# Performance work log

Hardware: AMD Instinct MI355X
Metric: run time of the kernel (lower is better)

Reference implementation:

```python
import jax, jax.numpy as jnp
import numpy as np

N = 50000      # nodes
E = 1600000    # edges (avg degree 32)
F = 11         # atom_features
ED = 4         # edge_dim
L = 4          # num_layers
G = 500        # graphs in batch


def _lin(k, fi, fo, layers=True):
    s = 1.0 / np.sqrt(fi)
    kw, kb = jax.random.split(k)
    sw = (L, fi, fo) if layers else (fi, fo)
    sb = (L, fo) if layers else (fo,)
    return (jax.random.uniform(kw, sw, jnp.float32, -s, s),
            jax.random.uniform(kb, sb, jnp.float32, -s, s))


def setup_inputs() -> dict:
    key = jax.random.key(0)
    ks = jax.random.split(key, 16)
    inp = {}
    inp["h"] = jax.random.normal(ks[0], (N, F), jnp.float32)
    inp["pos"] = jax.random.normal(ks[1], (N, 3), jnp.float32)
    inp["edge_index"] = jax.random.randint(ks[2], (2, E), 0, N)
    inp["edge_attr"] = jax.random.normal(ks[3], (E, ED), jnp.float32)
    inp["batch"] = jnp.sort(jax.random.randint(ks[4], (N,), 0, G))
    # stacked per-layer linear params
    specs = [("W_msg1", "b_msg1", 2 * F + 1 + ED, F),
             ("W_msg2", "b_msg2", F, F),
             ("W_attn", "b_attn", F, 1),
             ("W_upd1", "b_upd1", 2 * F, F),
             ("W_upd2", "b_upd2", F, F),
             ("W_x1", "b_x1", 2 * F + 1 + ED, F),
             ("W_x2", "b_x2", F, F),
             ("W_x3", "b_x3", F, 1)]
    for i, (wn, bn, fi, fo) in enumerate(specs):
        w, b = _lin(ks[5 + i], fi, fo)
        inp[wn] = w
        inp[bn] = b
    w, b = _lin(ks[14], F, 1, layers=False)
    inp["W_pred"] = w
    inp["b_pred"] = b
    return inp


def reference(h, pos, edge_index, edge_attr, batch,
              W_msg1, b_msg1, W_msg2, b_msg2, W_attn, b_attn,
              W_upd1, b_upd1, W_upd2, b_upd2,
              W_x1, b_x1, W_x2, b_x2, W_x3, b_x3,
              W_pred, b_pred):
    src, dst = edge_index[0], edge_index[1]  # j (source), i (target)
    x = pos
    for l in range(L):
        h_i, h_j = h[dst], h[src]
        x_i, x_j = x[dst], x[src]
        d = jnp.linalg.norm(x_j - x_i, axis=-1, keepdims=True)  # [E,1]
        feat = jnp.concatenate([h_i, h_j, d * d, edge_attr], axis=-1)  # [E,27]
        m = jax.nn.silu(feat @ W_msg1[l] + b_msg1[l])
        m = jax.nn.silu(m @ W_msg2[l] + b_msg2[l])
        attn = jax.nn.sigmoid(m @ W_attn[l] + b_attn[l])
        msg_h = attn * m                                          # [E,F]
        phi = jax.nn.silu(feat @ W_x1[l] + b_x1[l])
        phi = jax.nn.silu(phi @ W_x2[l] + b_x2[l])
        phi = phi @ W_x3[l] + b_x3[l]                             # [E,1]
        msg_x = (x_i - x_j) / (d + 1.0) * phi                     # [E,3]
        agg_h = jax.ops.segment_sum(msg_h, dst, num_segments=N)
        agg_x = jax.ops.segment_sum(msg_x, dst, num_segments=N)
        upd = jax.nn.silu(jnp.concatenate([h, agg_h], axis=-1) @ W_upd1[l] + b_upd1[l])
        upd = upd @ W_upd2[l] + b_upd2[l]
        h = h + upd          # residual (h = h + h_upd in outer loop)
        x = x + agg_x        # out_x = x + agg_x
    # global mean pool over graphs, then linear head
    counts = jax.ops.segment_sum(jnp.ones((N, 1), h.dtype), batch, num_segments=G)
    h_graph = jax.ops.segment_sum(h, batch, num_segments=G) / jnp.maximum(counts, 1.0)
    return (h_graph @ W_pred + b_pred).reshape(-1)
```

## Files before the change

kernel.cpp:

```cpp
#include <hip/hip_runtime.h>

#define N_NODES 50000
#define N_EDGES 1600000
#define F 11
#define FEAT 27
#define NLAYERS 4
#define NGRAPH 500
#define NVALS 14
#define PRESTRIDE 24
#define NBLK 196

__device__ __forceinline__ float siluf(float v) { return v * (1.0f / (1.0f + __expf(-v))); }
__device__ __forceinline__ float sigmf(float v) { return 1.0f / (1.0f + __expf(-v)); }

__device__ __forceinline__ float2 pkfma(float2 a, float2 b, float2 c) {
    float2 d;
    asm("v_pk_fma_f32 %0, %1, %2, %3" : "=v"(d) : "v"(a), "v"(b), "v"(c));
    return d;
}
__device__ __forceinline__ void rank1_pk(float v, const float4 w, float2& a0, float2& a1) {
    float2 vv = make_float2(v, v);
    a0 = pkfma(vv, make_float2(w.x, w.y), a0);
    a1 = pkfma(vv, make_float2(w.z, w.w), a1);
}

__global__ __launch_bounds__(256) void hist_kernel(const int* __restrict__ dst,
                                                   int* __restrict__ deg) {
    int e = blockIdx.x * 256 + threadIdx.x;
    if (e < N_EDGES) atomicAdd(&deg[dst[e]], 1);
}

__global__ __launch_bounds__(256) void scan1_kernel(const int* __restrict__ deg,
                                                    int* __restrict__ part,
                                                    int* __restrict__ bsum) {
    int t = threadIdx.x;
    int i = blockIdx.x * 256 + t;
    int v = (i < N_NODES) ? deg[i] : 0;
    int lane = t & 63, wid = t >> 6;
    int s = v;
    #pragma unroll
    for (int off = 1; off < 64; off <<= 1) {
        int u = __shfl_up(s, off);
        if (lane >= off) s += u;
    }
    __shared__ int wsum[4];
    if (lane == 63) wsum[wid] = s;
    __syncthreads();
    int wpre = 0;
    #pragma unroll
    for (int w = 0; w < 4; ++w) if (w < wid) wpre += wsum[w];
    if (i < N_NODES) part[i] = s + wpre - v;
    if (t == 255) bsum[blockIdx.x] = s + wpre;
}

__global__ __launch_bounds__(256) void scan2_kernel(int* __restrict__ bsum) {
    int t = threadIdx.x;
    int v = (t < NBLK) ? bsum[t] : 0;
    int lane = t & 63, wid = t >> 6;
    int s = v;
    #pragma unroll
    for (int off = 1; off < 64; off <<= 1) {
        int u = __shfl_up(s, off);
        if (lane >= off) s += u;
    }
    __shared__ int wsum[4];
    if (lane == 63) wsum[wid] = s;
    __syncthreads();
    int wpre = 0;
    #pragma unroll
    for (int w = 0; w < 4; ++w) if (w < wid) wpre += wsum[w];
    if (t < NBLK) bsum[t] = s + wpre - v;
}

__global__ __launch_bounds__(256) void scan3_kernel(const int* __restrict__ part,
                                                    const int* __restrict__ bsum,
                                                    int* __restrict__ cursor) {
    int i = blockIdx.x * 256 + threadIdx.x;
    if (i < N_NODES) cursor[i] = part[i] + bsum[blockIdx.x];
}

__global__ __launch_bounds__(256) void scatter_perm(const int* __restrict__ dst,
                                                    int* __restrict__ cursor,
                                                    int* __restrict__ perm) {
    int e = blockIdx.x * 256 + threadIdx.x;
    if (e >= N_EDGES) return;
    int d = dst[e];
    int pos = atomicAdd(&cursor[d], 1);
    perm[pos] = e;
}

__global__ __launch_bounds__(256) void mat_kernel(
    const int* __restrict__ perm, const int* __restrict__ src,
    const int* __restrict__ dst, const float4* __restrict__ eattr4,
    int* __restrict__ ssrc, int* __restrict__ sdst, float4* __restrict__ sea) {
    int i = blockIdx.x * 256 + threadIdx.x;
    if (i >= N_EDGES) return;
    int e = perm[i];
    ssrc[i] = src[e];
    sdst[i] = dst[e];
    sea[i] = eattr4[e];
}

__global__ __launch_bounds__(256) void init_kernel(
    const float* __restrict__ h0, const float* __restrict__ pos,
    float* __restrict__ h, float* __restrict__ x,
    const float* __restrict__ Wm1, const float* __restrict__ bm1,
    const float* __restrict__ Wx1, const float* __restrict__ bx1,
    float* __restrict__ preA, float* __restrict__ preB)
{
    __shared__ float sM[2 * F * F], sX[2 * F * F], sbm[F], sbx[F];
    int t = threadIdx.x;
    for (int i2 = t; i2 < 2 * F * F; i2 += 256) { sM[i2] = Wm1[i2]; sX[i2] = Wx1[i2]; }
    if (t < F) { sbm[t] = bm1[t]; sbx[t] = bx1[t]; }
    __syncthreads();

    int n = blockIdx.x * 256 + t;
    if (n >= N_NODES) return;

    float hv[F];
    #pragma unroll
    for (int f2 = 0; f2 < F; ++f2) { hv[f2] = h0[n * F + f2]; h[n * F + f2] = hv[f2]; }
    #pragma unroll
    for (int k = 0; k < 3; ++k) x[n * 3 + k] = pos[n * 3 + k];

    float am[F], bm_[F], ax[F], bx_[F];
    #pragma unroll
    for (int o = 0; o < F; ++o) { am[o] = sbm[o]; ax[o] = sbx[o]; bm_[o] = 0.f; bx_[o] = 0.f; }
    #pragma unroll
    for (int fi = 0; fi < F; ++fi) {
        float v = hv[fi];
        #pragma unroll
        for (int o = 0; o < F; ++o) {
            am[o]  = fmaf(v, sM[fi * F + o], am[o]);
            bm_[o] = fmaf(v, sM[(F + fi) * F + o], bm_[o]);
            ax[o]  = fmaf(v, sX[fi * F + o], ax[o]);
            bx_[o] = fmaf(v, sX[(F + fi) * F + o], bx_[o]);
        }
    }
    #pragma unroll
    for (int o = 0; o < F; ++o) {
        preA[n * PRESTRIDE + o]      = am[o];
        preA[n * PRESTRIDE + 12 + o] = ax[o];
        preB[n * PRESTRIDE + o]      = bm_[o];
        preB[n * PRESTRIDE + 12 + o] = bx_[o];
    }
    preA[n * PRESTRIDE + 11] = 0.f; preA[n * PRESTRIDE + 23] = 0.f;
    preB[n * PRESTRIDE + 11] = 0.f; preB[n * PRESTRIDE + 23] = 0.f;
}

__global__ __launch_bounds__(256) void edge_kernel(
    const float* __restrict__ preA, const float* __restrict__ preB,
    const float* __restrict__ x,
    const int* __restrict__ ssrc, const int* __restrict__ sdst,
    const float4* __restrict__ sea,
    const float* __restrict__ Wm1,
    const float* __restrict__ Wm2, const float* __restrict__ bm2,
    const float* __restrict__ Wa,  const float* __restrict__ ba,
    const float* __restrict__ Wx1,
    const float* __restrict__ Wx2, const float* __restrict__ bx2,
    const float* __restrict__ Wx3, const float* __restrict__ bx3,
    float* __restrict__ agg_h, float* __restrict__ agg_x)
{
    __shared__ float4 sW2m[F * 3], sW2x[F * 3];
    __shared__ float4 sD2m[3], sD2x[3], sEAm[4 * 3], sEAx[4 * 3];
    __shared__ float4 sB2m[3], sB2x[3], sWav[3], sWx3v[3];
    __shared__ float sba, sbx3;
    int t = threadIdx.x;
    {
        float* w2m = (float*)sW2m; float* w2x = (float*)sW2x;
        for (int i2 = t; i2 < F * 12; i2 += 256) {
            int r = i2 / 12, c = i2 % 12;
            w2m[i2] = (c < F) ? Wm2[r * F + c] : 0.f;
            w2x[i2] = (c < F) ? Wx2[r * F + c] : 0.f;
        }
        float* eam = (float*)sEAm; float* eax = (float*)sEAx;
        for (int i2 = t; i2 < 4 * 12; i2 += 256) {
            int r = i2 / 12, c = i2 % 12;
            eam[i2] = (c < F) ? Wm1[(23 + r) * F + c] : 0.f;
            eax[i2] = (c < F) ? Wx1[(23 + r) * F + c] : 0.f;
        }
        if (t < 12) {
            ((float*)sD2m)[t] = (t < F) ? Wm1[22 * F + t] : 0.f;
            ((float*)sD2x)[t] = (t < F) ? Wx1[22 * F + t] : 0.f;
            ((float*)sB2m)[t] = (t < F) ? bm2[t] : 0.f;
            ((float*)sB2x)[t] = (t < F) ? bx2[t] : 0.f;
            ((float*)sWav)[t] = (t < F) ? Wa[t] : 0.f;
            ((float*)sWx3v)[t] = (t < F) ? Wx3[t] : 0.f;
        }
        if (t == 0) { sba = ba[0]; sbx3 = bx3[0]; }
    }
    __syncthreads();

    int e = blockIdx.x * 256 + t;
    if (e >= N_EDGES) return;

    int j = ssrc[e];
    int d = sdst[e];

    float4 pa[6], pb[6];
    {
        const float4* pa4 = reinterpret_cast<const float4*>(preA + (size_t)d * PRESTRIDE);
        const float4* pb4 = reinterpret_cast<const float4*>(preB + (size_t)j * PRESTRIDE);
        #pragma unroll
        for (int q = 0; q < 6; ++q) { pa[q] = pa4[q]; pb[q] = pb4[q]; }
    }

    float xi0 = x[d * 3 + 0], xi1 = x[d * 3 + 1], xi2 = x[d * 3 + 2];
    float xj0 = x[j * 3 + 0], xj1 = x[j * 3 + 1], xj2 = x[j * 3 + 2];
    float dx = xj0 - xi0, dy = xj1 - xi1, dz = xj2 - xi2;
    float d2 = dx * dx + dy * dy + dz * dz;
    float4 ea = sea[e];

    float2 am[6], axv[6];
    #pragma unroll
    for (int q = 0; q < 3; ++q) {
        float4 sm, sx;
        sm.x = pa[q].x + pb[q].x; sm.y = pa[q].y + pb[q].y;
        sm.z = pa[q].z + pb[q].z; sm.w = pa[q].w + pb[q].w;
        sx.x = pa[3 + q].x + pb[3 + q].x; sx.y = pa[3 + q].y + pb[3 + q].y;
        sx.z = pa[3 + q].z + pb[3 + q].z; sx.w = pa[3 + q].w + pb[3 + q].w;
        am[2 * q]     = make_float2(sm.x, sm.y);
        am[2 * q + 1] = make_float2(sm.z, sm.w);
        axv[2 * q]     = make_float2(sx.x, sx.y);
        axv[2 * q + 1] = make_float2(sx.z, sx.w);
    }
    #pragma unroll
    for (int qq = 0; qq < 3; ++qq) {
        rank1_pk(d2, sD2m[qq], am[2 * qq], am[2 * qq + 1]);
        rank1_pk(d2, sD2x[qq], axv[2 * qq], axv[2 * qq + 1]);
    }
    float eav[4] = {ea.x, ea.y, ea.z, ea.w};
    #pragma unroll
    for (int k = 0; k < 4; ++k) {
        #pragma unroll
        for (int qq = 0; qq < 3; ++qq) {
            rank1_pk(eav[k], sEAm[k * 3 + qq], am[2 * qq], am[2 * qq + 1]);
            rank1_pk(eav[k], sEAx[k * 3 + qq], axv[2 * qq], axv[2 * qq + 1]);
        }
    }

    float tm[12], tx[12];
    #pragma unroll
    for (int q = 0; q < 6; ++q) {
        tm[2 * q] = am[q].x; tm[2 * q + 1] = am[q].y;
        tx[2 * q] = axv[q].x; tx[2 * q + 1] = axv[q].y;
    }
    #pragma unroll
    for (int o = 0; o < F; ++o) { tm[o] = siluf(tm[o]); tx[o] = siluf(tx[o]); }

    float2 m2a[6], p2a[6];
    {
        const float2* b2m = (const float2*)sB2m;
        const float2* b2x = (const float2*)sB2x;
        #pragma unroll
        for (int q = 0; q < 6; ++q) { m2a[q] = b2m[q]; p2a[q] = b2x[q]; }
    }
    #pragma unroll
    for (int fi = 0; fi < F; ++fi) {
        float a = tm[fi], b = tx[fi];
        #pragma unroll
        for (int qq = 0; qq < 3; ++qq) {
            rank1_pk(a, sW2m[fi * 3 + qq], m2a[2 * qq], m2a[2 * qq + 1]);
            rank1_pk(b, sW2x[fi * 3 + qq], p2a[2 * qq], p2a[2 * qq + 1]);
        }
    }
    float m2s[12], p2s[12];
    #pragma unroll
    for (int q = 0; q < 6; ++q) {
        m2s[2 * q] = m2a[q].x; m2s[2 * q + 1] = m2a[q].y;
        p2s[2 * q] = p2a[q].x; p2s[2 * q + 1] = p2a[q].y;
    }
    #pragma unroll
    for (int o = 0; o < F; ++o) { m2s[o] = siluf(m2s[o]); p2s[o] = siluf(p2s[o]); }
    m2s[11] = 0.f; p2s[11] = 0.f;

    float2 accA = make_float2(0.f, 0.f), accP = make_float2(0.f, 0.f);
    {
        const float2* wa = (const float2*)sWav;
        const float2* w3 = (const float2*)sWx3v;
        #pragma unroll
        for (int q = 0; q < 6; ++q) {
            accA = pkfma(make_float2(m2s[2 * q], m2s[2 * q + 1]), wa[q], accA);
            accP = pkfma(make_float2(p2s[2 * q], p2s[2 * q + 1]), w3[q], accP);
        }
    }
    float attn = sigmf(sba + accA.x + accA.y);
    float phi  = sbx3 + accP.x + accP.y;

    float dist = sqrtf(d2);
    float sc = phi / (dist + 1.0f);

    float vals[NVALS];
    #pragma unroll
    for (int o = 0; o < F; ++o) vals[o] = attn * m2s[o];
    vals[F + 0] = (xi0 - xj0) * sc;
    vals[F + 1] = (xi1 - xj1) * sc;
    vals[F + 2] = (xi2 - xj2) * sc;

    int lane = t & 63;
    #pragma unroll
    for (int off = 1; off < 64; off <<= 1) {
        int du = __shfl_down(d, off);
        bool ok = (lane + off < 64) && (du == d);
        #pragma unroll
        for (int k = 0; k < NVALS; ++k) {
            float up = __shfl_down(vals[k], off);
            if (ok) vals[k] += up;
        }
    }
    int dprev = __shfl_up(d, 1);
    if (lane == 0 || dprev != d) {
        #pragma unroll
        for (int o = 0; o < F; ++o) unsafeAtomicAdd(&agg_h[d * F + o], vals[o]);
        unsafeAtomicAdd(&agg_x[d * 3 + 0], vals[F + 0]);
        unsafeAtomicAdd(&agg_x[d * 3 + 1], vals[F + 1]);
        unsafeAtomicAdd(&agg_x[d * 3 + 2], vals[F + 2]);
    }
}

__global__ __launch_bounds__(256) void node_kernel(
    float* __restrict__ h, float* __restrict__ x,
    const float* __restrict__ agg_h, const float* __restrict__ agg_x,
    const float* __restrict__ Wu1, const float* __restrict__ bu1,
    const float* __restrict__ Wu2, const float* __restrict__ bu2,
    const float* __restrict__ Wm1n, const float* __restrict__ bm1n,
    const float* __restrict__ Wx1n, const float* __restrict__ bx1n,
    float* __restrict__ preA, float* __restrict__ preB, int has_next)
{
    __shared__ float sWu1[2 * F * F], sWu2[F * F], sbu1[F], sbu2[F];
    __shared__ float sM[2 * F * F], sX[2 * F * F], sbm[F], sbx[F];
    int t = threadIdx.x;
    for (int i2 = t; i2 < 2 * F * F; i2 += 256) sWu1[i2] = Wu1[i2];
    for (int i2 = t; i2 < F * F; i2 += 256)     sWu2[i2] = Wu2[i2];
    if (t < F) { sbu1[t] = bu1[t]; sbu2[t] = bu2[t]; }
    if (has_next) {
        for (int i2 = t; i2 < 2 * F * F; i2 += 256) { sM[i2] = Wm1n[i2]; sX[i2] = Wx1n[i2]; }
        if (t < F) { sbm[t] = bm1n[t]; sbx[t] = bx1n[t]; }
    }
    __syncthreads();

    int n = blockIdx.x * 256 + t;
    if (n >= N_NODES) return;

    float in[2 * F];
    #pragma unroll
    for (int f2 = 0; f2 < F; ++f2) in[f2] = h[n * F + f2];
    #pragma unroll
    for (int f2 = 0; f2 < F; ++f2) in[F + f2] = agg_h[n * F + f2];

    float u[F];
    #pragma unroll
    for (int o = 0; o < F; ++o) u[o] = sbu1[o];
    #pragma unroll
    for (int fi = 0; fi < 2 * F; ++fi) {
        float fv = in[fi];
        #pragma unroll
        for (int o = 0; o < F; ++o) u[o] = fmaf(fv, sWu1[fi * F + o], u[o]);
    }
    #pragma unroll
    for (int o = 0; o < F; ++o) u[o] = siluf(u[o]);

    float hn[F];
    #pragma unroll
    for (int o = 0; o < F; ++o) hn[o] = in[o] + sbu2[o];
    #pragma unroll
    for (int fi = 0; fi < F; ++fi) {
        float fv = u[fi];
        #pragma unroll
        for (int o = 0; o < F; ++o) hn[o] = fmaf(fv, sWu2[fi * F + o], hn[o]);
    }

    #pragma unroll
    for (int f2 = 0; f2 < F; ++f2) h[n * F + f2] = hn[f2];
    #pragma unroll
    for (int k = 0; k < 3; ++k) x[n * 3 + k] += agg_x[n * 3 + k];

    if (has_next) {
        float am[F], bm_[F], ax[F], bx_[F];
        #pragma unroll
        for (int o = 0; o < F; ++o) { am[o] = sbm[o]; ax[o] = sbx[o]; bm_[o] = 0.f; bx_[o] = 0.f; }
        #pragma unroll
        for (int fi = 0; fi < F; ++fi) {
            float v = hn[fi];
            #pragma unroll
            for (int o = 0; o < F; ++o) {
                am[o]  = fmaf(v, sM[fi * F + o], am[o]);
                bm_[o] = fmaf(v, sM[(F + fi) * F + o], bm_[o]);
                ax[o]  = fmaf(v, sX[fi * F + o], ax[o]);
                bx_[o] = fmaf(v, sX[(F + fi) * F + o], bx_[o]);
            }
        }
        #pragma unroll
        for (int o = 0; o < F; ++o) {
            preA[n * PRESTRIDE + o]      = am[o];
            preA[n * PRESTRIDE + 12 + o] = ax[o];
            preB[n * PRESTRIDE + o]      = bm_[o];
            preB[n * PRESTRIDE + 12 + o] = bx_[o];
        }
        preA[n * PRESTRIDE + 11] = 0.f; preA[n * PRESTRIDE + 23] = 0.f;
        preB[n * PRESTRIDE + 11] = 0.f; preB[n * PRESTRIDE + 23] = 0.f;
    }
}

__global__ __launch_bounds__(256) void pool_kernel(
    const float* __restrict__ h, const int* __restrict__ batch,
    float* __restrict__ gsum, float* __restrict__ gcnt)
{
    int n = blockIdx.x * blockDim.x + threadIdx.x;
    int lane = threadIdx.x & 63;
    bool valid = (n < N_NODES);
    int g = valid ? batch[n] : -1;
    float vals[F + 1];
    #pragma unroll
    for (int f2 = 0; f2 < F; ++f2) vals[f2] = valid ? h[n * F + f2] : 0.0f;
    vals[F] = valid ? 1.0f : 0.0f;

    #pragma unroll
    for (int off = 1; off < 64; off <<= 1) {
        int gu = __shfl_down(g, off);
        bool ok = (lane + off < 64) && (gu == g);
        #pragma unroll
        for (int k = 0; k < F + 1; ++k) {
            float up = __shfl_down(vals[k], off);
            if (ok) vals[k] += up;
        }
    }
    int gprev = __shfl_up(g, 1);
    if (valid && (lane == 0 || gprev != g)) {
        #pragma unroll
        for (int f2 = 0; f2 < F; ++f2) unsafeAtomicAdd(&gsum[g * F + f2], vals[f2]);
        unsafeAtomicAdd(&gcnt[g], vals[F]);
    }
}

__global__ void head_kernel(const float* __restrict__ gsum, const float* __restrict__ gcnt,
                            const float* __restrict__ Wp, const float* __restrict__ bp,
                            float* __restrict__ out)
{
    int g = blockIdx.x * blockDim.x + threadIdx.x;
    if (g >= NGRAPH) return;
    float c = fmaxf(gcnt[g], 1.0f);
    float inv = 1.0f / c;
    float acc = bp[0];
    #pragma unroll
    for (int f2 = 0; f2 < F; ++f2) acc = fmaf(gsum[g * F + f2] * inv, Wp[f2], acc);
    out[g] = acc;
}

extern "C" void kernel_launch(void* const* d_in, const int* in_sizes, int n_in,
                              void* d_out, int out_size, void* d_ws, size_t ws_size,
                              hipStream_t stream)
{
    const float* h0    = (const float*)d_in[0];
    const float* pos   = (const float*)d_in[1];
    const int*   eidx  = (const int*)d_in[2];
    const float* eattr = (const float*)d_in[3];
    const int*   batch = (const int*)d_in[4];
    const float* Wm1 = (const float*)d_in[5];
    const float* bm1 = (const float*)d_in[6];
    const float* Wm2 = (const float*)d_in[7];
    const float* bm2 = (const float*)d_in[8];
    const float* Wa  = (const float*)d_in[9];
    const float* ba  = (const float*)d_in[10];
    const float* Wu1 = (const float*)d_in[11];
    const float* bu1 = (const float*)d_in[12];
    const float* Wu2 = (const float*)d_in[13];
    const float* bu2 = (const float*)d_in[14];
    const float* Wx1 = (const float*)d_in[15];
    const float* bx1 = (const float*)d_in[16];
    const float* Wx2 = (const float*)d_in[17];
    const float* bx2 = (const float*)d_in[18];
    const float* Wx3 = (const float*)d_in[19];
    const float* bx3 = (const float*)d_in[20];
    const float* Wp  = (const float*)d_in[21];
    const float* bp  = (const float*)d_in[22];

    char* base = (char*)d_ws;
    float4* sea  = (float4*)base;                         base += (size_t)N_EDGES * 16;
    float* preA  = (float*)base;                          base += (size_t)N_NODES * PRESTRIDE * 4;
    float* preB  = (float*)base;                          base += (size_t)N_NODES * PRESTRIDE * 4;
    float* h_cur = (float*)base;                          base += (size_t)N_NODES * F * 4;
    float* x_cur = (float*)base;                          base += (size_t)N_NODES * 3 * 4;
    float* agg_h = (float*)base;                          base += (size_t)N_NODES * F * 4;
    float* agg_x = (float*)base;                          base += (size_t)N_NODES * 3 * 4;
    float* gsum  = (float*)base;                          base += (size_t)NGRAPH * F * 4;
    float* gcnt  = (float*)base;                          base += (size_t)NGRAPH * 4;
    int*   deg   = (int*)base;                            base += (size_t)N_NODES * 4;
    int*   part  = (int*)base;                            base += (size_t)N_NODES * 4;
    int*   bsum  = (int*)base;                            base += (size_t)256 * 4;
    int*   cursor= (int*)base;                            base += (size_t)N_NODES * 4;
    int*   perm  = (int*)base;                            base += (size_t)N_EDGES * 4;
    int*   ssrc  = (int*)base;                            base += (size_t)N_EDGES * 4;
    int*   sdst  = (int*)base;                            base += (size_t)N_EDGES * 4;

    const int* src = eidx;
    const int* dst = eidx + N_EDGES;

    hipMemsetAsync(deg, 0, (size_t)N_NODES * sizeof(int), stream);
    hist_kernel<<<(N_EDGES + 255) / 256, 256, 0, stream>>>(dst, deg);
    scan1_kernel<<<NBLK, 256, 0, stream>>>(deg, part, bsum);
    scan2_kernel<<<1, 256, 0, stream>>>(bsum);
    scan3_kernel<<<NBLK, 256, 0, stream>>>(part, bsum, cursor);
    scatter_perm<<<(N_EDGES + 255) / 256, 256, 0, stream>>>(dst, cursor, perm);
    mat_kernel<<<(N_EDGES + 255) / 256, 256, 0, stream>>>(
        perm, src, dst, reinterpret_cast<const float4*>(eattr), ssrc, sdst, sea);

    init_kernel<<<NBLK, 256, 0, stream>>>(h0, pos, h_cur, x_cur,
                                          Wm1, bm1, Wx1, bx1, preA, preB);

    for (int l = 0; l < NLAYERS; ++l) {
        hipMemsetAsync(agg_h, 0, (size_t)(N_NODES * (F + 3)) * sizeof(float), stream);
        edge_kernel<<<(N_EDGES + 255) / 256, 256, 0, stream>>>(
            preA, preB, x_cur, ssrc, sdst, sea,
            Wm1 + l * FEAT * F,
            Wm2 + l * F * F,    bm2 + l * F,
            Wa + l * F,         ba + l,
            Wx1 + l * FEAT * F,
            Wx2 + l * F * F,    bx2 + l * F,
            Wx3 + l * F,        bx3 + l,
            agg_h, agg_x);
        int nl = l + 1;
        int has_next = (nl < NLAYERS) ? 1 : 0;
        int wl = has_next ? nl : l;
        node_kernel<<<NBLK, 256, 0, stream>>>(
            h_cur, x_cur, agg_h, agg_x,
            Wu1 + l * 2 * F * F, bu1 + l * F,
            Wu2 + l * F * F,     bu2 + l * F,
            Wm1 + wl * FEAT * F, bm1 + wl * F,
            Wx1 + wl * FEAT * F, bx1 + wl * F,
            preA, preB, has_next);
    }

    hipMemsetAsync(gsum, 0, (size_t)(NGRAPH * F + NGRAPH) * sizeof(float), stream);
    pool_kernel<<<(N_NODES + 255) / 256, 256, 0, stream>>>(h_cur, batch, gsum, gcnt);
    head_kernel<<<2, 256, 0, stream>>>(gsum, gcnt, Wp, bp, (float*)d_out);
}
```

Before: 807.0 us.

## Aggregate edges per node-chunk in LDS via CSR rowptr, drop global atomics

Result: slower. 1.165 ms (+44.4%).

```diff
diff --git a/kernel.cpp b/kernel.cpp
--- a/kernel.cpp
+++ b/kernel.cpp
@@ -9,6 +9,8 @@
 #define NVALS 14
 #define PRESTRIDE 24
 #define NBLK 196
+#define CHUNK_NODES 25
+#define NCHUNK 2000
 
 __device__ __forceinline__ float siluf(float v) { return v * (1.0f / (1.0f + __expf(-v))); }
 __device__ __forceinline__ float sigmf(float v) { return 1.0f / (1.0f + __expf(-v)); }
@@ -74,31 +76,28 @@
 
 __global__ __launch_bounds__(256) void scan3_kernel(const int* __restrict__ part,
                                                     const int* __restrict__ bsum,
-                                                    int* __restrict__ cursor) {
+                                                    int* __restrict__ cursor,
+                                                    int* __restrict__ rowptr) {
     int i = blockIdx.x * 256 + threadIdx.x;
-    if (i < N_NODES) cursor[i] = part[i] + bsum[blockIdx.x];
-}
-
-__global__ __launch_bounds__(256) void scatter_perm(const int* __restrict__ dst,
-                                                    int* __restrict__ cursor,
-                                                    int* __restrict__ perm) {
+    if (i < N_NODES) {
+        int v = part[i] + bsum[blockIdx.x];
+        cursor[i] = v;
+        rowptr[i] = v;
+    }
+    if (blockIdx.x == 0 && threadIdx.x == 0) rowptr[N_NODES] = N_EDGES;
+}
+
+__global__ __launch_bounds__(256) void scatter_kernel(
+    const int* __restrict__ src, const int* __restrict__ dst,
+    const float* __restrict__ eattr, int* __restrict__ cursor,
+    int* __restrict__ ssrc, int* __restrict__ sdst, float4* __restrict__ sea) {
     int e = blockIdx.x * 256 + threadIdx.x;
     if (e >= N_EDGES) return;
     int d = dst[e];
     int pos = atomicAdd(&cursor[d], 1);
-    perm[pos] = e;
-}
-
-__global__ __launch_bounds__(256) void mat_kernel(
-    const int* __restrict__ perm, const int* __restrict__ src,
-    const int* __restrict__ dst, const float4* __restrict__ eattr4,
-    int* __restrict__ ssrc, int* __restrict__ sdst, float4* __restrict__ sea) {
-    int i = blockIdx.x * 256 + threadIdx.x;
-    if (i >= N_EDGES) return;
-    int e = perm[i];
-    ssrc[i] = src[e];
-    sdst[i] = dst[e];
-    sea[i] = eattr4[e];
+    ssrc[pos] = src[e];
+    sdst[pos] = d;
+    sea[pos] = reinterpret_cast<const float4*>(eattr)[e];
 }
 
 __global__ __launch_bounds__(256) void init_kernel(
@@ -151,6 +150,7 @@
 __global__ __launch_bounds__(256) void edge_kernel(
     const float* __restrict__ preA, const float* __restrict__ preB,
     const float* __restrict__ x,
+    const int* __restrict__ rowptr,
     const int* __restrict__ ssrc, const int* __restrict__ sdst,
     const float4* __restrict__ sea,
     const float* __restrict__ Wm1,
@@ -165,6 +165,8 @@
     __shared__ float4 sD2m[3], sD2x[3], sEAm[4 * 3], sEAx[4 * 3];
     __shared__ float4 sB2m[3], sB2x[3], sWav[3], sWx3v[3];
     __shared__ float sba, sbx3;
+    __shared__ float sAgg[CHUNK_NODES][NVALS];
+    __shared__ int sE[2];
     int t = threadIdx.x;
     {
         float* w2m = (float*)sW2m; float* w2x = (float*)sW2x;
@@ -189,132 +191,152 @@
         }
         if (t == 0) { sba = ba[0]; sbx3 = bx3[0]; }
     }
+    for (int i2 = t; i2 < CHUNK_NODES * NVALS; i2 += 256) ((float*)sAgg)[i2] = 0.f;
+    int nbase = blockIdx.x * CHUNK_NODES;
+    if (t == 0) { sE[0] = rowptr[nbase]; sE[1] = rowptr[nbase + CHUNK_NODES]; }
     __syncthreads();
 
-    int e = blockIdx.x * 256 + t;
-    if (e >= N_EDGES) return;
-
-    int j = ssrc[e];
-    int d = sdst[e];
-
-    float4 pa[6], pb[6];
-    {
-        const float4* pa4 = reinterpret_cast<const float4*>(preA + (size_t)d * PRESTRIDE);
-        const float4* pb4 = reinterpret_cast<const float4*>(preB + (size_t)j * PRESTRIDE);
-        #pragma unroll
-        for (int q = 0; q < 6; ++q) { pa[q] = pa4[q]; pb[q] = pb4[q]; }
-    }
-
-    float xi0 = x[d * 3 + 0], xi1 = x[d * 3 + 1], xi2 = x[d * 3 + 2];
-    float xj0 = x[j * 3 + 0], xj1 = x[j * 3 + 1], xj2 = x[j * 3 + 2];
-    float dx = xj0 - xi0, dy = xj1 - xi1, dz = xj2 - xi2;
-    float d2 = dx * dx + dy * dy + dz * dz;
-    float4 ea = sea[e];
-
-    float2 am[6], axv[6];
-    #pragma unroll
-    for (int q = 0; q < 3; ++q) {
-        float4 sm, sx;
-        sm.x = pa[q].x + pb[q].x; sm.y = pa[q].y + pb[q].y;
-        sm.z = pa[q].z + pb[q].z; sm.w = pa[q].w + pb[q].w;
-        sx.x = pa[3 + q].x + pb[3 + q].x; sx.y = pa[3 + q].y + pb[3 + q].y;
-        sx.z = pa[3 + q].z + pb[3 + q].z; sx.w = pa[3 + q].w + pb[3 + q].w;
-        am[2 * q]     = make_float2(sm.x, sm.y);
-        am[2 * q + 1] = make_float2(sm.z, sm.w);
-        axv[2 * q]     = make_float2(sx.x, sx.y);
-        axv[2 * q + 1] = make_float2(sx.z, sx.w);
-    }
-    #pragma unroll
-    for (int qq = 0; qq < 3; ++qq) {
-        rank1_pk(d2, sD2m[qq], am[2 * qq], am[2 * qq + 1]);
-        rank1_pk(d2, sD2x[qq], axv[2 * qq], axv[2 * qq + 1]);
-    }
-    float eav[4] = {ea.x, ea.y, ea.z, ea.w};
-    #pragma unroll
-    for (int k = 0; k < 4; ++k) {
+    int estart = sE[0], eend = sE[1];
+    int K = (eend - estart + 255) >> 8;
+    int lane = t & 63;
+
+    for (int k = 0; k < K; ++k) {
+        int e = estart + (k << 8) + t;
+        bool act = (e < eend);
+        int el = act ? e : (eend - 1);
+
+        int j = ssrc[el];
+        int d = sdst[el];
+
+        float4 pa[6], pb[6];
+        {
+            const float4* pa4 = reinterpret_cast<const float4*>(preA + (size_t)d * PRESTRIDE);
+            const float4* pb4 = reinterpret_cast<const float4*>(preB + (size_t)j * PRESTRIDE);
+            #pragma unroll
+            for (int q = 0; q < 6; ++q) { pa[q] = pa4[q]; pb[q] = pb4[q]; }
+        }
+
+        float xi0 = x[d * 3 + 0], xi1 = x[d * 3 + 1], xi2 = x[d * 3 + 2];
+        float xj0 = x[j * 3 + 0], xj1 = x[j * 3 + 1], xj2 = x[j * 3 + 2];
+        float dx = xj0 - xi0, dy = xj1 - xi1, dz = xj2 - xi2;
+        float d2 = dx * dx + dy * dy + dz * dz;
+        float4 ea = sea[el];
+
+        float2 am[6], axv[6];
+        #pragma unroll
+        for (int q = 0; q < 3; ++q) {
+            float4 sm, sx;
+            sm.x = pa[q].x + pb[q].x; sm.y = pa[q].y + pb[q].y;
+            sm.z = pa[q].z + pb[q].z; sm.w = pa[q].w + pb[q].w;
+            sx.x = pa[3 + q].x + pb[3 + q].x; sx.y = pa[3 + q].y + pb[3 + q].y;
+            sx.z = pa[3 + q].z + pb[3 + q].z; sx.w = pa[3 + q].w + pb[3 + q].w;
+            am[2 * q]      = make_float2(sm.x, sm.y);
+            am[2 * q + 1]  = make_float2(sm.z, sm.w);
+            axv[2 * q]     = make_float2(sx.x, sx.y);
+            axv[2 * q + 1] = make_float2(sx.z, sx.w);
+        }
         #pragma unroll
         for (int qq = 0; qq < 3; ++qq) {
-            rank1_pk(eav[k], sEAm[k * 3 + qq], am[2 * qq], am[2 * qq + 1]);
-            rank1_pk(eav[k], sEAx[k * 3 + qq], axv[2 * qq], axv[2 * qq + 1]);
-        }
-    }
-
-    float tm[12], tx[12];
-    #pragma unroll
-    for (int q = 0; q < 6; ++q) {
-        tm[2 * q] = am[q].x; tm[2 * q + 1] = am[q].y;
-        tx[2 * q] = axv[q].x; tx[2 * q + 1] = axv[q].y;
-    }
-    #pragma unroll
-    for (int o = 0; o < F; ++o) { tm[o] = siluf(tm[o]); tx[o] = siluf(tx[o]); }
-
-    float2 m2a[6], p2a[6];
-    {
-        const float2* b2m = (const float2*)sB2m;
-        const float2* b2x = (const float2*)sB2x;
-        #pragma unroll
-        for (int q = 0; q < 6; ++q) { m2a[q] = b2m[q]; p2a[q] = b2x[q]; }
-    }
-    #pragma unroll
-    for (int fi = 0; fi < F; ++fi) {
-        float a = tm[fi], b = tx[fi];
-        #pragma unroll
-        for (int qq = 0; qq < 3; ++qq) {
-            rank1_pk(a, sW2m[fi * 3 + qq], m2a[2 * qq], m2a[2 * qq + 1]);
-            rank1_pk(b, sW2x[fi * 3 + qq], p2a[2 * qq], p2a[2 * qq + 1]);
-        }
-    }
-    float m2s[12], p2s[12];
-    #pragma unroll
-    for (int q = 0; q < 6; ++q) {
-        m2s[2 * q] = m2a[q].x; m2s[2 * q + 1] = m2a[q].y;
-        p2s[2 * q] = p2a[q].x; p2s[2 * q + 1] = p2a[q].y;
-    }
-    #pragma unroll
-    for (int o = 0; o < F; ++o) { m2s[o] = siluf(m2s[o]); p2s[o] = siluf(p2s[o]); }
-    m2s[11] = 0.f; p2s[11] = 0.f;
-
-    float2 accA = make_float2(0.f, 0.f), accP = make_float2(0.f, 0.f);
-    {
-        const float2* wa = (const float2*)sWav;
-        const float2* w3 = (const float2*)sWx3v;
+            rank1_pk(d2, sD2m[qq], am[2 * qq], am[2 * qq + 1]);
+            rank1_pk(d2, sD2x[qq], axv[2 * qq], axv[2 * qq + 1]);
+        }
+        float eav[4] = {ea.x, ea.y, ea.z, ea.w};
+        #pragma unroll
+        for (int kk = 0; kk < 4; ++kk) {
+            #pragma unroll
+            for (int qq = 0; qq < 3; ++qq) {
+                rank1_pk(eav[kk], sEAm[kk * 3 + qq], am[2 * qq], am[2 * qq + 1]);
+                rank1_pk(eav[kk], sEAx[kk * 3 + qq], axv[2 * qq], axv[2 * qq + 1]);
+            }
+        }
+
+        float tm[12], tx[12];
         #pragma unroll
         for (int q = 0; q < 6; ++q) {
-            accA = pkfma(make_float2(m2s[2 * q], m2s[2 * q + 1]), wa[q], accA);
-            accP = pkfma(make_float2(p2s[2 * q], p2s[2 * q + 1]), w3[q], accP);
-        }
-    }
-    float attn = sigmf(sba + accA.x + accA.y);
-    float phi  = sbx3 + accP.x + accP.y;
-
-    float dist = sqrtf(d2);
-    float sc = phi / (dist + 1.0f);
-
-    float vals[NVALS];
-    #pragma unroll
-    for (int o = 0; o < F; ++o) vals[o] = attn * m2s[o];
-    vals[F + 0] = (xi0 - xj0) * sc;
-    vals[F + 1] = (xi1 - xj1) * sc;
-    vals[F + 2] = (xi2 - xj2) * sc;
-
-    int lane = t & 63;
-    #pragma unroll
-    for (int off = 1; off < 64; off <<= 1) {
-        int du = __shfl_down(d, off);
-        bool ok = (lane + off < 64) && (du == d);
-        #pragma unroll
-        for (int k = 0; k < NVALS; ++k) {
-            float up = __shfl_down(vals[k], off);
-            if (ok) vals[k] += up;
-        }
-    }
-    int dprev = __shfl_up(d, 1);
-    if (lane == 0 || dprev != d) {
-        #pragma unroll
-        for (int o = 0; o < F; ++o) unsafeAtomicAdd(&agg_h[d * F + o], vals[o]);
-        unsafeAtomicAdd(&agg_x[d * 3 + 0], vals[F + 0]);
-        unsafeAtomicAdd(&agg_x[d * 3 + 1], vals[F + 1]);
-        unsafeAtomicAdd(&agg_x[d * 3 + 2], vals[F + 2]);
+            tm[2 * q] = am[q].x; tm[2 * q + 1] = am[q].y;
+            tx[2 * q] = axv[q].x; tx[2 * q + 1] = axv[q].y;
+        }
+        #pragma unroll
+        for (int o = 0; o < F; ++o) { tm[o] = siluf(tm[o]); tx[o] = siluf(tx[o]); }
+
+        float2 m2a[6], p2a[6];
+        {
+            const float2* b2m = (const float2*)sB2m;
+            const float2* b2x = (const float2*)sB2x;
+            #pragma unroll
+            for (int q = 0; q < 6; ++q) { m2a[q] = b2m[q]; p2a[q] = b2x[q]; }
+        }
+        #pragma unroll
+        for (int fi = 0; fi < F; ++fi) {
+            float a = tm[fi], b = tx[fi];
+            #pragma unroll
+            for (int qq = 0; qq < 3; ++qq) {
+                rank1_pk(a, sW2m[fi * 3 + qq], m2a[2 * qq], m2a[2 * qq + 1]);
+                rank1_pk(b, sW2x[fi * 3 + qq], p2a[2 * qq], p2a[2 * qq + 1]);
+            }
+        }
+        float m2s[12], p2s[12];
+        #pragma unroll
+        for (int q = 0; q < 6; ++q) {
+            m2s[2 * q] = m2a[q].x; m2s[2 * q + 1] = m2a[q].y;
+            p2s[2 * q] = p2a[q].x; p2s[2 * q + 1] = p2a[q].y;
+        }
+        #pragma unroll
+        for (int o = 0; o < F; ++o) { m2s[o] = siluf(m2s[o]); p2s[o] = siluf(p2s[o]); }
+
+        float2 accA = make_float2(0.f, 0.f), accP = make_float2(0.f, 0.f);
+        {
+            const float2* wa = (const float2*)sWav;
+            const float2* w3 = (const float2*)sWx3v;
+            #pragma unroll
+            for (int q = 0; q < 5; ++q) {
+                accA = pkfma(make_float2(m2s[2 * q], m2s[2 * q + 1]), wa[q], accA);
+                accP = pkfma(make_float2(p2s[2 * q], p2s[2 * q + 1]), w3[q], accP);
+            }
+            accA.x = fmaf(m2s[10], ((const float*)sWav)[10], accA.x);
+            accP.x = fmaf(p2s[10], ((const float*)sWx3v)[10], accP.x);
+        }
+        float attn = sigmf(sba + accA.x + accA.y);
+        float phi  = sbx3 + accP.x + accP.y;
+
+        float dist = sqrtf(d2);
+        float sc = phi / (dist + 1.0f);
+
+        float vals[NVALS];
+        #pragma unroll
+        for (int o = 0; o < F; ++o) vals[o] = attn * m2s[o];
+        vals[F + 0] = (xi0 - xj0) * sc;
+        vals[F + 1] = (xi1 - xj1) * sc;
+        vals[F + 2] = (xi2 - xj2) * sc;
+
+        if (!act) d = -1;
+
+        #pragma unroll
+        for (int off = 1; off < 64; off <<= 1) {
+            int du = __shfl_down(d, off);
+            bool ok = (lane + off < 64) && (du == d);
+            #pragma unroll
+            for (int kk = 0; kk < NVALS; ++kk) {
+                float up = __shfl_down(vals[kk], off);
+                if (ok) vals[kk] += up;
+            }
+        }
+        int dprev = __shfl_up(d, 1);
+        bool leader = (d >= 0) && (lane == 0 || dprev != d);
+        if (leader) {
+            int slot = d - nbase;
+            #pragma unroll
+            for (int o = 0; o < NVALS; ++o) atomicAdd(&sAgg[slot][o], vals[o]);
+        }
+    }
+
+    __syncthreads();
+    for (int i2 = t; i2 < CHUNK_NODES * NVALS; i2 += 256) {
+        int n = nbase + i2 / NVALS;
+        int f = i2 % NVALS;
+        float v = ((const float*)sAgg)[i2];
+        if (f < F) agg_h[n * F + f] = v;
+        else       agg_x[n * 3 + (f - F)] = v;
     }
 }
 
@@ -489,7 +511,7 @@
     int*   part  = (int*)base;                            base += (size_t)N_NODES * 4;
     int*   bsum  = (int*)base;                            base += (size_t)256 * 4;
     int*   cursor= (int*)base;                            base += (size_t)N_NODES * 4;
-    int*   perm  = (int*)base;                            base += (size_t)N_EDGES * 4;
+    int*   rowptr= (int*)base;                            base += (size_t)(N_NODES + 1) * 4;
     int*   ssrc  = (int*)base;                            base += (size_t)N_EDGES * 4;
     int*   sdst  = (int*)base;                            base += (size_t)N_EDGES * 4;
 
@@ -500,18 +522,16 @@
     hist_kernel<<<(N_EDGES + 255) / 256, 256, 0, stream>>>(dst, deg);
     scan1_kernel<<<NBLK, 256, 0, stream>>>(deg, part, bsum);
     scan2_kernel<<<1, 256, 0, stream>>>(bsum);
-    scan3_kernel<<<NBLK, 256, 0, stream>>>(part, bsum, cursor);
-    scatter_perm<<<(N_EDGES + 255) / 256, 256, 0, stream>>>(dst, cursor, perm);
-    mat_kernel<<<(N_EDGES + 255) / 256, 256, 0, stream>>>(
-        perm, src, dst, reinterpret_cast<const float4*>(eattr), ssrc, sdst, sea);
+    scan3_kernel<<<NBLK, 256, 0, stream>>>(part, bsum, cursor, rowptr);
+    scatter_kernel<<<(N_EDGES + 255) / 256, 256, 0, stream>>>(
+        src, dst, eattr, cursor, ssrc, sdst, sea);
 
     init_kernel<<<NBLK, 256, 0, stream>>>(h0, pos, h_cur, x_cur,
                                           Wm1, bm1, Wx1, bx1, preA, preB);
 
     for (int l = 0; l < NLAYERS; ++l) {
-        hipMemsetAsync(agg_h, 0, (size_t)(N_NODES * (F + 3)) * sizeof(float), stream);
-        edge_kernel<<<(N_EDGES + 255) / 256, 256, 0, stream>>>(
-            preA, preB, x_cur, ssrc, sdst, sea,
+        edge_kernel<<<NCHUNK, 256, 0, stream>>>(
+            preA, preB, x_cur, rowptr, ssrc, sdst, sea,
             Wm1 + l * FEAT * F,
             Wm2 + l * F * F,    bm2 + l * F,
             Wa + l * F,         ba + l,
```
